# Kernel tuning notes

Hardware: AMD Instinct MI355X
Metric: run time of the kernel (lower is better)

## Reference

```python
import jax, jax.numpy as jnp
import numpy as np

B, L, S, D, H, DH = 32, 96, 96, 512, 8, 64  # d_ff = S*S = 9216


def setup_inputs() -> dict:
    key = jax.random.key(0)
    ks = jax.random.split(key, 13)
    sc = 0.02
    inp = {
        "queries": jax.random.normal(ks[0], (B, L, D), jnp.float32),
        "keys": jax.random.normal(ks[1], (B, S, D), jnp.float32),
        "values": jax.random.normal(ks[2], (B, S, D), jnp.float32),
        "attn_mask": jnp.zeros((B, L, S), dtype=bool),
        # projections stored as (in, out); torch Linear is x @ W.T + b
        "Wq": jax.random.normal(ks[3], (D, H * DH), jnp.float32) * sc,
        "bq": jnp.zeros((H * DH,), jnp.float32),
        "Wk": jax.random.normal(ks[4], (D, H * DH), jnp.float32) * sc,
        "bk": jnp.zeros((H * DH,), jnp.float32),
        "Wv": jax.random.normal(ks[5], (D, H * DH), jnp.float32) * sc,
        "bv": jnp.zeros((H * DH,), jnp.float32),
        # core_value initialized as softmax over rank dim, as in the module
        "core": jax.nn.softmax(jax.random.normal(ks[6], (H, DH), jnp.float32), axis=-1),
        "Wo": jax.random.normal(ks[7], (S * S, D), jnp.float32) * sc,
        "bo": jnp.zeros((D,), jnp.float32),
    }
    return inp


def reference(queries, keys, values, attn_mask, Wq, bq, Wk, bk, Wv, bv, core, Wo, bo):
    b, l, _ = queries.shape
    s = keys.shape[1]
    h, d = core.shape
    # NOTE: the original uses .view(H, B, L, -1) on a (B, L, H*d) tensor —
    # a raw reshape, NOT a transpose. Replicate faithfully.
    q = (queries @ Wq + bq).reshape(h, b, l, d)
    k = (keys @ Wk + bk).reshape(h, b, s, d)
    v = (values @ Wv + bv).reshape(h, b, s, d)
    # per-head rank-d CP contraction, summed over heads, averaged by 1/H
    full = jnp.einsum("nh,nbih,nbjh,nbkh->bijk", core, q, k, v) / h  # [B,L,S,S]
    full = full.reshape(b, l, s * s)
    out = full @ Wo + bo  # [B, L, D]
    return out
```

## Files before the change

kernel.cpp:

```cpp
#include <hip/hip_runtime.h>
#include <hip/hip_bf16.h>
#include <stdint.h>

using bf16 = __hip_bfloat16;
typedef float v4f __attribute__((ext_vector_type(4)));
typedef short short8 __attribute__((ext_vector_type(8)));


__device__ __forceinline__ void async_cp16(void* l, const void* g) {
  __builtin_amdgcn_global_load_lds(
      (const __attribute__((address_space(1))) void*)(uintptr_t)g,
      (__attribute__((address_space(3))) void*)(uintptr_t)l, 16, 0, 0);
}

__global__ __launch_bounds__(256) void prep(
    const float* __restrict__ Wo, const float* __restrict__ Wq,
    const float* __restrict__ Wk, const float* __restrict__ Wv,
    const float* __restrict__ Xq, const float* __restrict__ Xk,
    const float* __restrict__ Xv, const float* __restrict__ bo,
    bf16* __restrict__ WoT, bf16* __restrict__ WTq,
    bf16* __restrict__ WTk, bf16* __restrict__ WTv,
    bf16* __restrict__ Xbq, bf16* __restrict__ Xbk, bf16* __restrict__ Xbv,
    float* __restrict__ out) {
  const int bid = blockIdx.x, t = threadIdx.x;
  if (bid < 5376) {
    __shared__ bf16 T[32][33];
    const float* src; bf16* dst; int K, N, kx, ny;
    if (bid < 4608) {
      src = Wo; dst = WoT; K = 9216; N = 512; kx = bid % 288; ny = bid / 288;
    } else {
      const int r = bid - 4608, which = r >> 8, rr = r & 255;
      kx = rr & 15; ny = rr >> 4; K = 512; N = 512;
      src = which == 0 ? Wq : (which == 1 ? Wk : Wv);
      dst = which == 0 ? WTq : (which == 1 ? WTk : WTv);
    }
    const int k0 = kx * 32, n0 = ny * 32;
    const int r = t >> 3, c = (t & 7) * 4;
    float4 v = *reinterpret_cast<const float4*>(src + (size_t)(k0 + r) * N + n0 + c);
    T[c + 0][r] = __float2bfloat16(v.x);
    T[c + 1][r] = __float2bfloat16(v.y);
    T[c + 2][r] = __float2bfloat16(v.z);
    T[c + 3][r] = __float2bfloat16(v.w);
    __syncthreads();
    union { uint2 u; bf16 h[4]; } o;
    o.h[0] = T[r][c + 0]; o.h[1] = T[r][c + 1];
    o.h[2] = T[r][c + 2]; o.h[3] = T[r][c + 3];
    *reinterpret_cast<uint2*>(dst + (size_t)(n0 + r) * K + k0 + c) = o.u;
  } else if (bid < 6528) {
    const int r = bid - 5376;
    const int which = r / 384, blk = r % 384;
    const float* src = which == 0 ? Xq : (which == 1 ? Xk : Xv);
    bf16* dst = which == 0 ? Xbq : (which == 1 ? Xbk : Xbv);
    const int base = blk * 4096 + t * 16;
    float4 a = *reinterpret_cast<const float4*>(src + base);
    float4 b = *reinterpret_cast<const float4*>(src + base + 4);
    float4 c = *reinterpret_cast<const float4*>(src + base + 8);
    float4 d = *reinterpret_cast<const float4*>(src + base + 12);
    union { uint4 u; bf16 h[8]; } o1, o2;
    o1.h[0] = __float2bfloat16(a.x); o1.h[1] = __float2bfloat16(a.y);
    o1.h[2] = __float2bfloat16(a.z); o1.h[3] = __float2bfloat16(a.w);
    o1.h[4] = __float2bfloat16(b.x); o1.h[5] = __float2bfloat16(b.y);
    o1.h[6] = __float2bfloat16(b.z); o1.h[7] = __float2bfloat16(b.w);
    o2.h[0] = __float2bfloat16(c.x); o2.h[1] = __float2bfloat16(c.y);
    o2.h[2] = __float2bfloat16(c.z); o2.h[3] = __float2bfloat16(c.w);
    o2.h[4] = __float2bfloat16(d.x); o2.h[5] = __float2bfloat16(d.y);
    o2.h[6] = __float2bfloat16(d.z); o2.h[7] = __float2bfloat16(d.w);
    *reinterpret_cast<uint4*>(dst + base) = o1.u;
    *reinterpret_cast<uint4*>(dst + base + 8) = o2.u;
  } else {
    const int r = bid - 6528;
    const int idx = (r * 256 + t) * 4;
    *reinterpret_cast<float4*>(out + idx) =
        *reinterpret_cast<const float4*>(bo + (idx & 511));
  }
}

__global__ __launch_bounds__(256) void proj_mfma(
    const bf16* __restrict__ Xb0, const bf16* __restrict__ Xb1,
    const bf16* __restrict__ Xb2,
    const bf16* __restrict__ WT0, const bf16* __restrict__ WT1,
    const bf16* __restrict__ WT2,
    const float* __restrict__ b0, const float* __restrict__ b1,
    const float* __restrict__ b2, const float* __restrict__ core,
    bf16* __restrict__ O0, bf16* __restrict__ O1, bf16* __restrict__ O2) {
  const int z = blockIdx.z;
  const bf16* X    = z == 0 ? Xb0 : (z == 1 ? Xb1 : Xb2);
  const bf16* WT   = z == 0 ? WT0 : (z == 1 ? WT1 : WT2);
  const float* bia = z == 0 ? b0 : (z == 1 ? b1 : b2);
  bf16* O          = z == 0 ? O0 : (z == 1 ? O1 : O2);

  const int bm = blockIdx.x * 128, bn = blockIdx.y * 64;
  __shared__ __align__(16) bf16 As[128 * 128];
  __shared__ __align__(16) bf16 Bs[64 * 128];
  const int t = threadIdx.x;
  const int w = t >> 6, lane = t & 63;
  const int m16 = lane & 15, q = lane >> 4;
  const int l16 = lane >> 4, l15 = lane & 15;

  v4f acc[2][4] = {};

  for (int k0 = 0; k0 < 512; k0 += 128) {
    __syncthreads();
    #pragma unroll
    for (int c = 0; c < 8; c++) {
      const int row = (w * 8 + c) * 4 + l16;
      const int lch = l15 ^ (row & 7);
      async_cp16(&As[(w * 8 + c) * 512],
                 X + (size_t)(bm + row) * 512 + k0 + lch * 8);
    }
    #pragma unroll
    for (int c = 0; c < 4; c++) {
      const int row = (w * 4 + c) * 4 + l16;
      const int lch = l15 ^ (row & 7);
      async_cp16(&Bs[(w * 4 + c) * 512],
                 WT + (size_t)(bn + row) * 512 + k0 + lch * 8);
    }
    __syncthreads();

    #pragma unroll
    for (int s = 0; s < 4; s++) {
      const int pc = ((s * 4 + q) ^ (m16 & 7)) * 8;
      short8 af[2], bfr[4];
      #pragma unroll
      for (int mt = 0; mt < 2; mt++)
        af[mt] = *reinterpret_cast<const short8*>(
            &As[(w * 32 + mt * 16 + m16) * 128 + pc]);
      #pragma unroll
      for (int nt = 0; nt < 4; nt++)
        bfr[nt] = *reinterpret_cast<const short8*>(
            &Bs[(nt * 16 + m16) * 128 + pc]);
      #pragma unroll
      for (int mt = 0; mt < 2; mt++)
        #pragma unroll
        for (int nt = 0; nt < 4; nt++)
          acc[mt][nt] = __builtin_amdgcn_mfma_f32_16x16x32_bf16(
              af[mt], bfr[nt], acc[mt][nt], 0, 0, 0);
    }
  }

  const bool isQ = (z == 0);
  const int nblk = bm / 384;
  #pragma unroll
  for (int mt = 0; mt < 2; mt++)
    #pragma unroll
    for (int nt = 0; nt < 4; nt++)
      #pragma unroll
      for (int r = 0; r < 4; r++) {
        const int row = bm + w * 32 + mt * 16 + q * 4 + r;
        const int col = bn + nt * 16 + m16;
        float v = acc[mt][nt][r] + bia[col];
        if (isQ) v *= core[nblk * 64 + (col & 63)] * 0.125f;
        O[(size_t)row * 512 + col] = __float2bfloat16(v);
      }
}

__global__ __launch_bounds__(256) void stage_b_mfma(
    const bf16* __restrict__ AQ, const bf16* __restrict__ KPb,
    const bf16* __restrict__ VPb, bf16* __restrict__ FULL) {
  const int b = blockIdx.y;
  const int i0 = blockIdx.x * 2;

  __shared__ __align__(16) bf16 smem[19456];
  bf16* Ks0 = smem;
  bf16* Ks1 = smem + 6144;
  bf16* Vs  = smem + 12288;
  bf16* aqs = smem + 18432;

  const int t = threadIdx.x;
  const int w = t >> 6, lane = t & 63;
  const int wr = w >> 1, wc = w & 1;
  const int m16 = lane & 15, q = lane >> 4;
  const int l8 = lane >> 3, l7 = lane & 7;

  if (t < 128) {
    const int isel = t & 1, n = t >> 4, seg = (t >> 1) & 7;
    *reinterpret_cast<uint4*>(&aqs[isel * 512 + n * 64 + seg * 8]) =
        *reinterpret_cast<const uint4*>(
            AQ + (size_t)n * 196608 + b * 6144 + (i0 + isel) * 64 + seg * 8);
  }

  union U8 { uint4 u; bf16 h[8]; };
  const int colq = (t & 7) * 8;
  const int rowk = t >> 3;
  const int krow7 = rowk & 7;

  U8 kk[3];
  {
    const bf16* Kp = KPb + b * 6144;
    #pragma unroll
    for (int c3 = 0; c3 < 3; c3++)
      kk[c3].u = *reinterpret_cast<const uint4*>(Kp + (t + c3 * 256) * 8);
  }

  v4f acc[2][3][3] = {};

  for (int n = 0; n < 8; n++) {
    __syncthreads();
    const bf16* Vp = VPb + (size_t)n * 196608 + b * 6144;
    #pragma unroll
    for (int c = 0; c < 3; c++) {
      const int r0 = (w * 3 + c) * 8;
      async_cp16(&Vs[(w * 3 + c) * 512],
                 Vp + (r0 + l8) * 64 + (l7 ^ l8) * 8);
    }
    float a0f[8], a1f[8];
    {
      U8 a0, a1;
      a0.u = *reinterpret_cast<const uint4*>(&aqs[n * 64 + colq]);
      a1.u = *reinterpret_cast<const uint4*>(&aqs[512 + n * 64 + colq]);
      #pragma unroll
      for (int e = 0; e < 8; e++) {
        a0f[e] = __bfloat162float(a0.h[e]);
        a1f[e] = __bfloat162float(a1.h[e]);
      }
    }
    #pragma unroll
    for (int c3 = 0; c3 < 3; c3++) {
      U8 s0, s1;
      #pragma unroll
      for (int e = 0; e < 8; e++) {
        const float kv = __bfloat162float(kk[c3].h[e]);
        s0.h[e] = __float2bfloat16(kv * a0f[e]);
        s1.h[e] = __float2bfloat16(kv * a1f[e]);
      }
      const int phys = (rowk + 32 * c3) * 64 + (l7 ^ krow7) * 8;
      *reinterpret_cast<uint4*>(&Ks0[phys]) = s0.u;
      *reinterpret_cast<uint4*>(&Ks1[phys]) = s1.u;
    }
    __syncthreads();
    if (n < 7) {
      const bf16* Kp1 = KPb + (size_t)(n + 1) * 196608 + b * 6144;
      #pragma unroll
      for (int c3 = 0; c3 < 3; c3++)
        kk[c3].u = *reinterpret_cast<const uint4*>(Kp1 + (t + c3 * 256) * 8);
    }

    #pragma unroll
    for (int s = 0; s < 2; s++) {
      const int pc = ((s * 4 + q) ^ (m16 & 7)) * 8;
      short8 bfr[3], af0[3], af1[3];
      #pragma unroll
      for (int cc = 0; cc < 3; cc++)
        bfr[cc] = *reinterpret_cast<const short8*>(
            &Vs[(wc * 48 + cc * 16 + m16) * 64 + pc]);
      #pragma unroll
      for (int a = 0; a < 3; a++) {
        af0[a] = *reinterpret_cast<const short8*>(
            &Ks0[(wr * 48 + a * 16 + m16) * 64 + pc]);
        af1[a] = *reinterpret_cast<const short8*>(
            &Ks1[(wr * 48 + a * 16 + m16) * 64 + pc]);
      }
      #pragma unroll
      for (int a = 0; a < 3; a++)
        #pragma unroll
        for (int cc = 0; cc < 3; cc++) {
          acc[0][a][cc] = __builtin_amdgcn_mfma_f32_16x16x32_bf16(
              af0[a], bfr[cc], acc[0][a][cc], 0, 0, 0);
          acc[1][a][cc] = __builtin_amdgcn_mfma_f32_16x16x32_bf16(
              af1[a], bfr[cc], acc[1][a][cc], 0, 0, 0);
        }
    }
  }

  __syncthreads();
  #pragma unroll
  for (int isel = 0; isel < 2; isel++)
    #pragma unroll
    for (int a = 0; a < 3; a++)
      #pragma unroll
      for (int cc = 0; cc < 3; cc++) {
        const int j0 = wr * 48 + a * 16, k0c = wc * 48 + cc * 16;
        #pragma unroll
        for (int r = 0; r < 4; r++)
          smem[isel * 9216 + (j0 + q * 4 + r) * 96 + k0c + m16] =
              __float2bfloat16(acc[isel][a][cc][r]);
      }
  __syncthreads();
  const size_t obase = (size_t)(b * 96 + i0) * 9216;
  #pragma unroll
  for (int c = t; c < 2304; c += 256)
    *reinterpret_cast<uint4*>(FULL + obase + c * 8) =
        *reinterpret_cast<const uint4*>(&smem[c * 8]);
}

__global__ __launch_bounds__(256) void stage_c_mfma(
    const bf16* __restrict__ FULL, const bf16* __restrict__ WoT,
    float* __restrict__ out) {
  const int bm = blockIdx.x * 128, bn = blockIdx.y * 64;
  const int kbase = blockIdx.z * 2304;
  __shared__ __align__(16) bf16 As[2][128 * 64];
  __shared__ __align__(16) bf16 Bs[2][64 * 64];
  const int t = threadIdx.x;
  const int w = t >> 6, lane = t & 63;
  const int m16 = lane & 15, q = lane >> 4;
  const int l8 = lane >> 3, l7 = lane & 7;

  v4f acc[2][4] = {};

#define SC_STAGE(buf, k0)                                                    \
  {                                                                          \
    _Pragma("unroll")                                                        \
    for (int c = 0; c < 4; c++) {                                            \
      const int r0 = (w * 4 + c) * 8;                                        \
      async_cp16(&As[buf][(w * 4 + c) * 512],                                \
                 FULL + (size_t)(bm + r0 + l8) * 9216 + (k0) + (l7 ^ l8) * 8); \
    }                                                                        \
    _Pragma("unroll")                                                        \
    for (int c = 0; c < 2; c++) {                                            \
      const int r0 = (w * 2 + c) * 8;                                        \
      async_cp16(&Bs[buf][(w * 2 + c) * 512],                                \
                 WoT + (size_t)(bn + r0 + l8) * 9216 + (k0) + (l7 ^ l8) * 8);  \
    }                                                                        \
  }

#define SC_COMPUTE(buf)                                                      \
  {                                                                          \
    _Pragma("unroll")                                                        \
    for (int s = 0; s < 2; s++) {                                            \
      const int pc = ((s * 4 + q) ^ (m16 & 7)) * 8;                          \
      short8 af[2], bfr[4];                                                  \
      _Pragma("unroll")                                                      \
      for (int mt = 0; mt < 2; mt++)                                         \
        af[mt] = *reinterpret_cast<const short8*>(                           \
            &As[buf][(w * 32 + mt * 16 + m16) * 64 + pc]);                   \
      _Pragma("unroll")                                                      \
      for (int nt = 0; nt < 4; nt++)                                         \
        bfr[nt] = *reinterpret_cast<const short8*>(                          \
            &Bs[buf][(nt * 16 + m16) * 64 + pc]);                            \
      _Pragma("unroll")                                                      \
      for (int mt = 0; mt < 2; mt++)                                         \
        _Pragma("unroll")                                                    \
        for (int nt = 0; nt < 4; nt++)                                       \
          acc[mt][nt] = __builtin_amdgcn_mfma_f32_16x16x32_bf16(             \
              af[mt], bfr[nt], acc[mt][nt], 0, 0, 0);                        \
    }                                                                        \
  }

  SC_STAGE(0, kbase);
  __syncthreads();

  for (int it = 0; it < 18; it++) {
    SC_STAGE(1, kbase + (2 * it + 1) * 64);
    SC_COMPUTE(0);
    __syncthreads();
    if (it < 17) SC_STAGE(0, kbase + (2 * it + 2) * 64);
    SC_COMPUTE(1);
    __syncthreads();
  }

  #pragma unroll
  for (int mt = 0; mt < 2; mt++)
    #pragma unroll
    for (int nt = 0; nt < 4; nt++)
      #pragma unroll
      for (int r = 0; r < 4; r++) {
        const int row = bm + w * 32 + mt * 16 + q * 4 + r;
        const int col = bn + nt * 16 + m16;
        atomicAdd(&out[(size_t)row * 512 + col], acc[mt][nt][r]);
      }
#undef SC_STAGE
#undef SC_COMPUTE
}

extern "C" void kernel_launch(void* const* d_in, const int* in_sizes, int n_in,
                              void* d_out, int out_size, void* d_ws, size_t ws_size,
                              hipStream_t stream) {
  const float* queries = (const float*)d_in[0];
  const float* keys    = (const float*)d_in[1];
  const float* values  = (const float*)d_in[2];
  const float* Wq   = (const float*)d_in[4];
  const float* bq   = (const float*)d_in[5];
  const float* Wk   = (const float*)d_in[6];
  const float* bk   = (const float*)d_in[7];
  const float* Wv   = (const float*)d_in[8];
  const float* bv   = (const float*)d_in[9];
  const float* core = (const float*)d_in[10];
  const float* Wo   = (const float*)d_in[11];
  const float* bo   = (const float*)d_in[12];
  float* out = (float*)d_out;

  char* ws = (char*)d_ws;
  bf16* AQb = (bf16*)(ws);
  bf16* KPb = (bf16*)(ws + 3145728);
  bf16* VPb = (bf16*)(ws + 6291456);
  bf16* WTq = (bf16*)(ws + 9437184);
  bf16* WTk = (bf16*)(ws + 9961472);
  bf16* WTv = (bf16*)(ws + 10485760);
  bf16* WoT = (bf16*)(ws + 11010048);
  bf16* FULL = (bf16*)(ws + 20447232);
  bf16* Xbq = FULL;
  bf16* Xbk = FULL + 1572864;
  bf16* Xbv = FULL + 3145728;

  prep<<<dim3(8064), dim3(256), 0, stream>>>(
      Wo, Wq, Wk, Wv, queries, keys, values, bo,
      WoT, WTq, WTk, WTv, Xbq, Xbk, Xbv, out);

  proj_mfma<<<dim3(24, 8, 3), dim3(256), 0, stream>>>(
      Xbq, Xbk, Xbv, WTq, WTk, WTv, bq, bk, bv, core, AQb, KPb, VPb);

  stage_b_mfma<<<dim3(48, 32), dim3(256), 0, stream>>>(AQb, KPb, VPb, FULL);

  stage_c_mfma<<<dim3(24, 8, 4), dim3(256), 0, stream>>>(FULL, WoT, out);
}
```

Before: 202.6 us.

## Double-buffer projection GEMM with smaller tiles and widen prep transpose tiles

The projection GEMM moves to 64x64 tiles with 128 threads and a two-stage LDS double buffer, so async global-to-LDS loads of the next K slice overlap the MFMA work on the current one. The grid doubles to give more blocks. The weight transpose in prep now handles 64x32 tiles with 16-byte stores instead of 8-byte ones, halving the number of transpose blocks. In exchange each GEMM block has less data reuse, and the padded transpose tile may cause LDS bank conflicts.

New measurement: 201.9 us. About the same (-0.4%).

```diff
diff --git a/kernel.cpp b/kernel.cpp
--- a/kernel.cpp
+++ b/kernel.cpp
@@ -23,31 +23,31 @@
     bf16* __restrict__ Xbq, bf16* __restrict__ Xbk, bf16* __restrict__ Xbv,
     float* __restrict__ out) {
   const int bid = blockIdx.x, t = threadIdx.x;
-  if (bid < 5376) {
-    __shared__ bf16 T[32][33];
+  if (bid < 2688) {
+    __shared__ bf16 T[32][80];
     const float* src; bf16* dst; int K, N, kx, ny;
-    if (bid < 4608) {
-      src = Wo; dst = WoT; K = 9216; N = 512; kx = bid % 288; ny = bid / 288;
+    if (bid < 2304) {
+      src = Wo; dst = WoT; K = 9216; N = 512; kx = bid % 144; ny = bid / 144;
     } else {
-      const int r = bid - 4608, which = r >> 8, rr = r & 255;
-      kx = rr & 15; ny = rr >> 4; K = 512; N = 512;
+      const int r = bid - 2304, which = r >> 7, rr = r & 127;
+      kx = rr & 7; ny = rr >> 3; K = 512; N = 512;
       src = which == 0 ? Wq : (which == 1 ? Wk : Wv);
       dst = which == 0 ? WTq : (which == 1 ? WTk : WTv);
     }
-    const int k0 = kx * 32, n0 = ny * 32;
-    const int r = t >> 3, c = (t & 7) * 4;
-    float4 v = *reinterpret_cast<const float4*>(src + (size_t)(k0 + r) * N + n0 + c);
-    T[c + 0][r] = __float2bfloat16(v.x);
-    T[c + 1][r] = __float2bfloat16(v.y);
-    T[c + 2][r] = __float2bfloat16(v.z);
-    T[c + 3][r] = __float2bfloat16(v.w);
-    __syncthreads();
-    union { uint2 u; bf16 h[4]; } o;
-    o.h[0] = T[r][c + 0]; o.h[1] = T[r][c + 1];
-    o.h[2] = T[r][c + 2]; o.h[3] = T[r][c + 3];
-    *reinterpret_cast<uint2*>(dst + (size_t)(n0 + r) * K + k0 + c) = o.u;
-  } else if (bid < 6528) {
-    const int r = bid - 5376;
+    const int k0 = kx * 64, n0 = ny * 32;
+    const int kr = t >> 2, nc = (t & 3) * 8;
+    float4 v0 = *reinterpret_cast<const float4*>(src + (size_t)(k0 + kr) * N + n0 + nc);
+    float4 v1 = *reinterpret_cast<const float4*>(src + (size_t)(k0 + kr) * N + n0 + nc + 4);
+    T[nc + 0][kr] = __float2bfloat16(v0.x); T[nc + 1][kr] = __float2bfloat16(v0.y);
+    T[nc + 2][kr] = __float2bfloat16(v0.z); T[nc + 3][kr] = __float2bfloat16(v0.w);
+    T[nc + 4][kr] = __float2bfloat16(v1.x); T[nc + 5][kr] = __float2bfloat16(v1.y);
+    T[nc + 6][kr] = __float2bfloat16(v1.z); T[nc + 7][kr] = __float2bfloat16(v1.w);
+    __syncthreads();
+    const int n = t >> 3, kc = (t & 7) * 8;
+    *reinterpret_cast<uint4*>(dst + (size_t)(n0 + n) * K + k0 + kc) =
+        *reinterpret_cast<const uint4*>(&T[n][kc]);
+  } else if (bid < 3840) {
+    const int r = bid - 2688;
     const int which = r / 384, blk = r % 384;
     const float* src = which == 0 ? Xq : (which == 1 ? Xk : Xv);
     bf16* dst = which == 0 ? Xbq : (which == 1 ? Xbk : Xbv);
@@ -68,14 +68,14 @@
     *reinterpret_cast<uint4*>(dst + base) = o1.u;
     *reinterpret_cast<uint4*>(dst + base + 8) = o2.u;
   } else {
-    const int r = bid - 6528;
+    const int r = bid - 3840;
     const int idx = (r * 256 + t) * 4;
     *reinterpret_cast<float4*>(out + idx) =
         *reinterpret_cast<const float4*>(bo + (idx & 511));
   }
 }
 
-__global__ __launch_bounds__(256) void proj_mfma(
+__global__ __launch_bounds__(128) void proj_mfma(
     const bf16* __restrict__ Xb0, const bf16* __restrict__ Xb1,
     const bf16* __restrict__ Xb2,
     const bf16* __restrict__ WT0, const bf16* __restrict__ WT1,
@@ -89,54 +89,63 @@
   const float* bia = z == 0 ? b0 : (z == 1 ? b1 : b2);
   bf16* O          = z == 0 ? O0 : (z == 1 ? O1 : O2);
 
-  const int bm = blockIdx.x * 128, bn = blockIdx.y * 64;
-  __shared__ __align__(16) bf16 As[128 * 128];
-  __shared__ __align__(16) bf16 Bs[64 * 128];
+  const int bm = blockIdx.x * 64, bn = blockIdx.y * 64;
+  __shared__ __align__(16) bf16 As[2][64 * 64];
+  __shared__ __align__(16) bf16 Bs[2][64 * 64];
   const int t = threadIdx.x;
   const int w = t >> 6, lane = t & 63;
   const int m16 = lane & 15, q = lane >> 4;
-  const int l16 = lane >> 4, l15 = lane & 15;
+  const int l8 = lane >> 3, l7 = lane & 7;
 
   v4f acc[2][4] = {};
 
-  for (int k0 = 0; k0 < 512; k0 += 128) {
-    __syncthreads();
-    #pragma unroll
-    for (int c = 0; c < 8; c++) {
-      const int row = (w * 8 + c) * 4 + l16;
-      const int lch = l15 ^ (row & 7);
-      async_cp16(&As[(w * 8 + c) * 512],
-                 X + (size_t)(bm + row) * 512 + k0 + lch * 8);
-    }
-    #pragma unroll
-    for (int c = 0; c < 4; c++) {
-      const int row = (w * 4 + c) * 4 + l16;
-      const int lch = l15 ^ (row & 7);
-      async_cp16(&Bs[(w * 4 + c) * 512],
-                 WT + (size_t)(bn + row) * 512 + k0 + lch * 8);
-    }
-    __syncthreads();
-
-    #pragma unroll
-    for (int s = 0; s < 4; s++) {
-      const int pc = ((s * 4 + q) ^ (m16 & 7)) * 8;
-      short8 af[2], bfr[4];
-      #pragma unroll
-      for (int mt = 0; mt < 2; mt++)
-        af[mt] = *reinterpret_cast<const short8*>(
-            &As[(w * 32 + mt * 16 + m16) * 128 + pc]);
-      #pragma unroll
-      for (int nt = 0; nt < 4; nt++)
-        bfr[nt] = *reinterpret_cast<const short8*>(
-            &Bs[(nt * 16 + m16) * 128 + pc]);
-      #pragma unroll
-      for (int mt = 0; mt < 2; mt++)
-        #pragma unroll
-        for (int nt = 0; nt < 4; nt++)
-          acc[mt][nt] = __builtin_amdgcn_mfma_f32_16x16x32_bf16(
-              af[mt], bfr[nt], acc[mt][nt], 0, 0, 0);
-    }
-  }
+#define PJ_STAGE(buf, k0)                                                    \
+  {                                                                          \
+    _Pragma("unroll")                                                        \
+    for (int c = 0; c < 4; c++) {                                            \
+      const int r0 = (w * 4 + c) * 8;                                        \
+      async_cp16(&As[buf][(w * 4 + c) * 512],                                \
+                 X + (size_t)(bm + r0 + l8) * 512 + (k0) + (l7 ^ l8) * 8);   \
+      async_cp16(&Bs[buf][(w * 4 + c) * 512],                                \
+                 WT + (size_t)(bn + r0 + l8) * 512 + (k0) + (l7 ^ l8) * 8);  \
+    }                                                                        \
+  }
+
+#define PJ_COMPUTE(buf)                                                      \
+  {                                                                          \
+    _Pragma("unroll")                                                        \
+    for (int s = 0; s < 2; s++) {                                            \
+      const int pc = ((s * 4 + q) ^ (m16 & 7)) * 8;                          \
+      short8 af[2], bfr[4];                                                  \
+      _Pragma("unroll")                                                      \
+      for (int mt = 0; mt < 2; mt++)                                         \
+        af[mt] = *reinterpret_cast<const short8*>(                           \
+            &As[buf][(w * 32 + mt * 16 + m16) * 64 + pc]);                   \
+      _Pragma("unroll")                                                      \
+      for (int nt = 0; nt < 4; nt++)                                         \
+        bfr[nt] = *reinterpret_cast<const short8*>(                          \
+            &Bs[buf][(nt * 16 + m16) * 64 + pc]);                            \
+      _Pragma("unroll")                                                      \
+      for (int mt = 0; mt < 2; mt++)                                         \
+        _Pragma("unroll")                                                    \
+        for (int nt = 0; nt < 4; nt++)                                       \
+          acc[mt][nt] = __builtin_amdgcn_mfma_f32_16x16x32_bf16(             \
+              af[mt], bfr[nt], acc[mt][nt], 0, 0, 0);                        \
+    }                                                                        \
+  }
+
+  PJ_STAGE(0, 0);
+  __syncthreads();
+  for (int it = 0; it < 4; it++) {
+    PJ_STAGE(1, (2 * it + 1) * 64);
+    PJ_COMPUTE(0);
+    __syncthreads();
+    if (it < 3) PJ_STAGE(0, (2 * it + 2) * 64);
+    PJ_COMPUTE(1);
+    __syncthreads();
+  }
+#undef PJ_STAGE
+#undef PJ_COMPUTE
 
   const bool isQ = (z == 0);
   const int nblk = bm / 384;
@@ -392,11 +401,11 @@
   bf16* Xbk = FULL + 1572864;
   bf16* Xbv = FULL + 3145728;
 
-  prep<<<dim3(8064), dim3(256), 0, stream>>>(
+  prep<<<dim3(5376), dim3(256), 0, stream>>>(
       Wo, Wq, Wk, Wv, queries, keys, values, bo,
       WoT, WTq, WTk, WTv, Xbq, Xbk, Xbv, out);
 
-  proj_mfma<<<dim3(24, 8, 3), dim3(256), 0, stream>>>(
+  proj_mfma<<<dim3(48, 8, 3), dim3(128), 0, stream>>>(
       Xbq, Xbk, Xbv, WTq, WTk, WTv, bq, bk, bv, core, AQb, KPb, VPb);
 
   stage_b_mfma<<<dim3(48, 32), dim3(256), 0, stream>>>(AQb, KPb, VPb, FULL);
```
